# Optimization experiments

Measured on AMD Instinct MI355X. Metric: run time of the kernel, lower is better.

Reference implementation:

```python
import jax, jax.numpy as jnp
import numpy as np

BATCH = 4096
IN_CAPS = 64
OUT_CAPS = 16
IN_DIM = 64
OUT_DIM = 64
NUM_ITER = 3
LN_EPS = 1e-5


def setup_inputs() -> dict:
    key = jax.random.key(0)
    ks = jax.random.split(key, 13)
    n = lambda k, s: jax.random.normal(k, s, dtype=jnp.float32)
    return {
        "x_inp": n(ks[0], (BATCH, IN_CAPS, IN_DIM)),
        "W_A": n(ks[1], (IN_CAPS, IN_DIM)),
        "B_A": n(ks[2], (IN_CAPS,)),
        "W_F1": n(ks[3], (IN_CAPS, IN_DIM, IN_DIM)),
        "W_F2": n(ks[4], (OUT_CAPS, IN_DIM, OUT_DIM)),
        "B_F2": n(ks[5], (OUT_CAPS, OUT_DIM)),
        "W_G1": n(ks[6], (OUT_DIM, OUT_DIM)),
        "W_G2": n(ks[7], (OUT_CAPS, OUT_DIM, IN_DIM)),
        "B_G2": n(ks[8], (OUT_CAPS, IN_DIM)),
        "ln_gamma": jnp.ones((OUT_DIM,), jnp.float32),
        "ln_beta": jnp.zeros((OUT_DIM,), jnp.float32),
        "W_S": n(ks[9], (IN_CAPS, OUT_CAPS, IN_DIM)),
        "B_S": n(ks[10], (IN_CAPS, OUT_CAPS)),
        "beta_use": n(ks[11], (IN_CAPS, OUT_CAPS)),
        "beta_ign": n(ks[12], (IN_CAPS, OUT_CAPS)),
    }


def _layer_norm(x, gamma, beta):
    mu = jnp.mean(x, axis=-1, keepdims=True)
    var = jnp.var(x, axis=-1, keepdims=True)  # biased, matches torch LayerNorm
    return (x - mu) * jax.lax.rsqrt(var + LN_EPS) * gamma + beta


def reference(x_inp, W_A, B_A, W_F1, W_F2, B_F2, W_G1, W_G2, B_G2,
              ln_gamma, ln_beta, W_S, B_S, beta_use, beta_ign):
    B = x_inp.shape[0]
    inv_sqrt = np.float32(1.0 / np.sqrt(IN_DIM))
    # activation logits per input capsule: [B, in_caps]
    a_e = jnp.einsum('bif,if->bi', x_inp, W_A) * inv_sqrt + B_A
    f_a_e = jax.nn.sigmoid(a_e)  # loop-invariant
    # temp_F is loop-invariant: [B, in_caps, in_dim]
    temp_F = jnp.einsum('bif,ifh->bih', x_inp, W_F1) * inv_sqrt
    R_em = jnp.full((B, IN_CAPS, OUT_CAPS), 1.0 / OUT_CAPS, dtype=x_inp.dtype)
    x_out = None
    for _ in range(NUM_ITER):
        D_use = f_a_e[:, :, None] * R_em                      # [B,i,m]
        D_ign = f_a_e[:, :, None] - D_use                     # [B,i,m]
        phi_em = beta_use * D_use - beta_ign * D_ign          # [B,i,m]
        temp_F_routed = phi_em.sum(axis=-1)[:, :, None] * temp_F  # [B,i,h]
        x_out = jnp.einsum('bih,mhd->bmd', temp_F_routed, W_F2) + B_F2  # [B,m,d]
        x_out_norm = _layer_norm(x_out, ln_gamma, ln_beta)
        temp_G = jnp.einsum('bmd,dh->bmh', x_out_norm, W_G1)  # [B,m,d]
        x_inp_hat = jnp.einsum('bmh,mhi->bmi', temp_G, W_G2) + B_G2  # [B,m,f]
        consistency = jnp.einsum('bif,bmf,imf->bim', x_inp, x_inp_hat, W_S) + B_S
        R_em = jax.nn.softmax(consistency, axis=-1)  # exp(log_softmax)
    return x_out
```

## Files before the change

kernel.cpp:

```cpp
#include <hip/hip_runtime.h>
#include <math.h>

#define IC 64
#define OC 16
#define DIM 64

typedef __attribute__((ext_vector_type(8))) short bf16x8;
typedef __attribute__((ext_vector_type(4))) float f32x4;

__device__ __forceinline__ unsigned short f2bf(float f) {
    unsigned int b = __float_as_uint(f);
    b += 0x7fffu + ((b >> 16) & 1u);
    return (unsigned short)(b >> 16);
}
__device__ __forceinline__ float bf2f(unsigned short h) {
    return __uint_as_float(((unsigned int)h) << 16);
}

__global__ __launch_bounds__(256, 4)
void kF1(const float* __restrict__ W_F2, const float* __restrict__ W_S,
         const float* __restrict__ B_S, const float* __restrict__ bu,
         const float* __restrict__ bi_, const float* __restrict__ W_G1,
         const float* __restrict__ W_G2, const float* __restrict__ W_F1,
         const float* __restrict__ x, const float* __restrict__ W_A,
         const float* __restrict__ B_A,
         float* __restrict__ WSt2,
         unsigned short* __restrict__ W1h, unsigned short* __restrict__ W1l,
         unsigned short* __restrict__ W2h, unsigned short* __restrict__ W2l,
         unsigned short* __restrict__ WF1Th, unsigned short* __restrict__ WF1Tl,
         float* __restrict__ BSt, float* __restrict__ cb, float* __restrict__ db,
         float* __restrict__ xq, float* __restrict__ fa, float* __restrict__ phi)
{
    if (blockIdx.x < 256) {
        int e = blockIdx.x * 256 + threadIdx.x;
        {
            int h = e >> 10, m = (e >> 6) & 15, d = e & 63;
            float v = W_F2[((size_t)m * 64 + h) * 64 + d];
            unsigned short hh = f2bf(v);
            size_t o = ((size_t)m * 64 + d) * 64 + h;
            W1h[o] = hh; W1l[o] = f2bf(v - bf2f(hh));
        }
        {
            int m = e >> 12, fo = (e >> 8) & 15, i = (e >> 2) & 63, fi = e & 3;
            WSt2[e] = W_S[((size_t)i * 16 + m) * 64 + fo * 4 + fi];
        }
        {
            int m = e >> 12, d = (e >> 6) & 63, f = e & 63;
            const float* g1 = W_G1 + d * 64;
            const float* g2 = W_G2 + (size_t)m * 4096 + f;
            float a = 0.f;
#pragma unroll 8
            for (int h = 0; h < 64; h++) a += g1[h] * g2[h * 64];
            unsigned short hh = f2bf(a);
            size_t o = ((size_t)m * 64 + f) * 64 + d;
            W2h[o] = hh; W2l[o] = f2bf(a - bf2f(hh));
        }
        {
#pragma unroll
            for (int r = 0; r < 4; r++) {
                int idx = r * 65536 + e;
                int i = idx >> 12, h = (idx >> 6) & 63, f = idx & 63;
                float v = W_F1[(((size_t)i * 64 + f) * 64) + h];
                unsigned short hh = f2bf(v);
                size_t o = ((size_t)i * 64 + h) * 64 + f;
                WF1Th[o] = hh; WF1Tl[o] = f2bf(v - bf2f(hh));
            }
        }
        if (e < 1024) {
            int m = e >> 6, i = e & 63;
            BSt[e] = B_S[i * 16 + m];
            cb[e] = bu[e] + bi_[e];
        }
        if (e < 64) {
            float sd = 0.f;
            for (int m = 0; m < 16; m++) sd += bi_[e * 16 + m];
            db[e] = sd;
        }
        return;
    }

    __shared__ float Xs[2 * 64 * 65];
    const int t = threadIdx.x;
    const int blk = blockIdx.x - 256;

    const float4* x4 = (const float4*)x;
#pragma unroll
    for (int s = 0; s < 8; s++) {
        int p = s * 256 + t;
        float4 v = x4[(size_t)blk * 2048 + p];
        int b = p >> 10, i = (p >> 4) & 63, fo = p & 15;
        float* row = &Xs[(b * 64 + i) * 65 + fo * 4];
        row[0] = v.x; row[1] = v.y; row[2] = v.z; row[3] = v.w;
    }
    __syncthreads();

    const int lane = t & 63, w = t >> 6;
#pragma unroll
    for (int s = 0; s < 8; s++) {
        int idx = s * 4 + w;
        int b = idx >> 4, fo = idx & 15;
        const float* row = &Xs[(b * 64 + lane) * 65 + fo * 4];
        ((float4*)xq)[((size_t)(blk * 2 + b) * 16 + fo) * 64 + lane] =
            make_float4(row[0], row[1], row[2], row[3]);
    }

    {
        int p = t >> 1, h = t & 1;
        int b = p >> 6, i = p & 63;
        const float* row = &Xs[(b * 64 + i) * 65 + h * 32];
        const float* wa = W_A + i * 64 + h * 32;
        float v = 0.f;
#pragma unroll
        for (int j = 0; j < 32; j++) v += row[j] * wa[j];
        v += __shfl_xor(v, 1);
        if (h == 0) {
            float sc = 0.f, sd = 0.f;
            for (int m = 0; m < 16; m++) {
                float vu = bu[i * 16 + m], vi = bi_[i * 16 + m];
                sc += vu + vi; sd += vi;
            }
            float ebi = sc * (1.0f / 16.0f) - sd;
            float ae = v * 0.125f + B_A[i];
            float fv = 1.0f / (1.0f + expf(-ae));
            size_t o = (size_t)(blk * 2 + b) * 64 + i;
            fa[o] = fv;
            phi[o] = fv * ebi;
        }
    }
}

__global__ __launch_bounds__(256, 4)
void kA(const float* __restrict__ x,
        const unsigned short* __restrict__ WF1Th, const unsigned short* __restrict__ WF1Tl,
        float* __restrict__ tF)
{
    __shared__ unsigned short Ah[64][72], Al[64][72];
    __shared__ unsigned short Bh[64][72], Bl[64][72];
    const int i = blockIdx.y;
    const int b0 = blockIdx.x * 64;
    const int t = threadIdx.x;
    const int bl = t >> 2, q = t & 3;

    {
        const float* src = x + ((size_t)(b0 + bl) * IC + i) * DIM + q * 4;
#pragma unroll
        for (int j4 = 0; j4 < 4; j4++) {
            float4 v = *(const float4*)(src + j4 * 16);
            int f = q * 4 + j4 * 16;
            float vv[4] = {v.x, v.y, v.z, v.w};
            ushort4 h4, l4;
            unsigned short hh;
            hh = f2bf(vv[0]); h4.x = hh; l4.x = f2bf(vv[0] - bf2f(hh));
            hh = f2bf(vv[1]); h4.y = hh; l4.y = f2bf(vv[1] - bf2f(hh));
            hh = f2bf(vv[2]); h4.z = hh; l4.z = f2bf(vv[2] - bf2f(hh));
            hh = f2bf(vv[3]); h4.w = hh; l4.w = f2bf(vv[3] - bf2f(hh));
            *(ushort4*)&Ah[bl][f] = h4;
            *(ushort4*)&Al[bl][f] = l4;
        }
        const size_t wo = ((size_t)i * 64 + bl) * 64 + q * 16;
#pragma unroll
        for (int part = 0; part < 2; part++) {
            *(uint4*)&Bh[bl][q * 16 + part * 8] = *(const uint4*)(WF1Th + wo + part * 8);
            *(uint4*)&Bl[bl][q * 16 + part * 8] = *(const uint4*)(WF1Tl + wo + part * 8);
        }
    }
    __syncthreads();

    const int w = t >> 6, lane = t & 63;
    const int fm = lane & 15, fq = lane >> 4;
    const int r0 = w * 16;
    f32x4 acc[4];
#pragma unroll
    for (int nt = 0; nt < 4; nt++) {
        acc[nt][0] = 0.f; acc[nt][1] = 0.f; acc[nt][2] = 0.f; acc[nt][3] = 0.f;
    }

#pragma unroll
    for (int ks = 0; ks < 2; ks++) {
        const int kk = ks * 32 + fq * 8;
        bf16x8 ah = *(const bf16x8*)&Ah[r0 + fm][kk];
        bf16x8 al = *(const bf16x8*)&Al[r0 + fm][kk];
#pragma unroll
        for (int nt = 0; nt < 4; nt++) {
            bf16x8 bh = *(const bf16x8*)&Bh[nt * 16 + fm][kk];
            bf16x8 bl2 = *(const bf16x8*)&Bl[nt * 16 + fm][kk];
            acc[nt] = __builtin_amdgcn_mfma_f32_16x16x32_bf16(ah, bh, acc[nt], 0, 0, 0);
            acc[nt] = __builtin_amdgcn_mfma_f32_16x16x32_bf16(ah, bl2, acc[nt], 0, 0, 0);
            acc[nt] = __builtin_amdgcn_mfma_f32_16x16x32_bf16(al, bh, acc[nt], 0, 0, 0);
        }
    }

#pragma unroll
    for (int nt = 0; nt < 4; nt++)
#pragma unroll
        for (int j = 0; j < 4; j++) {
            int row = r0 + fq * 4 + j;
            int col = nt * 16 + fm;
            tF[((size_t)(b0 + row) * IC + i) * DIM + col] = acc[nt][j] * 0.125f;
        }
}

__global__ __launch_bounds__(256, 4)
void kS(const float* __restrict__ phi, const float* __restrict__ tF,
        float* __restrict__ s)
{
    __shared__ float ph[4 * 64];
    const int t = threadIdx.x;
    const int b0 = blockIdx.x * 4;
    ph[t] = phi[(size_t)b0 * 64 + t];
    __syncthreads();

    const int w = t >> 6, lane = t & 63;
    const int ig = lane >> 4, hq = lane & 15;
    const int b = b0 + w;
    const float4* tf4 = (const float4*)(tF + ((size_t)b * 64 + ig * 16) * 64) + hq;
    float4 a = make_float4(0.f, 0.f, 0.f, 0.f);
#pragma unroll
    for (int k = 0; k < 16; k++) {
        float p = ph[w * 64 + ig * 16 + k];
        float4 v = tf4[k * 16];
        a.x += p * v.x; a.y += p * v.y; a.z += p * v.z; a.w += p * v.w;
    }
#pragma unroll
    for (int k = 16; k <= 32; k <<= 1) {
        a.x += __shfl_xor(a.x, k); a.y += __shfl_xor(a.y, k);
        a.z += __shfl_xor(a.z, k); a.w += __shfl_xor(a.w, k);
    }
    if (ig == 0)
        ((float4*)(s + (size_t)b * 64))[hq] = a;
}

__global__ __launch_bounds__(256, 4)
void kXG(const float* __restrict__ s,
         const unsigned short* __restrict__ W1h, const unsigned short* __restrict__ W1l,
         const float* __restrict__ B_F2,
         const unsigned short* __restrict__ W2h, const unsigned short* __restrict__ W2l,
         const float* __restrict__ B_G2,
         const float* __restrict__ gam, const float* __restrict__ bet,
         float* __restrict__ xhat, float* __restrict__ out, const int last)
{
    __shared__ unsigned short Ah[64][72], Al[64][72];
    __shared__ unsigned short Bh[64][72], Bl[64][72];
    const int b0 = blockIdx.x * 64;
    const int m = blockIdx.y;
    const int t = threadIdx.x;
    const int bl = t >> 2, q = t & 3;

    {
        const float* src = s + (size_t)(b0 + bl) * DIM + q * 16;
#pragma unroll
        for (int j4 = 0; j4 < 4; j4++) {
            float4 v = ((const float4*)src)[j4];
            int f = q * 16 + j4 * 4;
            float vv[4] = {v.x, v.y, v.z, v.w};
            ushort4 h4, l4;
            unsigned short hh;
            hh = f2bf(vv[0]); h4.x = hh; l4.x = f2bf(vv[0] - bf2f(hh));
            hh = f2bf(vv[1]); h4.y = hh; l4.y = f2bf(vv[1] - bf2f(hh));
            hh = f2bf(vv[2]); h4.z = hh; l4.z = f2bf(vv[2] - bf2f(hh));
            hh = f2bf(vv[3]); h4.w = hh; l4.w = f2bf(vv[3] - bf2f(hh));
            *(ushort4*)&Ah[bl][f] = h4;
            *(ushort4*)&Al[bl][f] = l4;
        }
        const size_t wo = ((size_t)m * 64 + bl) * 64 + q * 16;
#pragma unroll
        for (int part = 0; part < 2; part++) {
            *(uint4*)&Bh[bl][q * 16 + part * 8] = *(const uint4*)(W1h + wo + part * 8);
            *(uint4*)&Bl[bl][q * 16 + part * 8] = *(const uint4*)(W1l + wo + part * 8);
        }
    }
    __syncthreads();

    const int w = t >> 6, lane = t & 63;
    const int fm = lane & 15, fq = lane >> 4;
    const int r0 = w * 16;
    f32x4 acc[4];
#pragma unroll
    for (int nt = 0; nt < 4; nt++) {
        acc[nt][0] = 0.f; acc[nt][1] = 0.f; acc[nt][2] = 0.f; acc[nt][3] = 0.f;
    }
#pragma unroll
    for (int ks = 0; ks < 2; ks++) {
        const int kk = ks * 32 + fq * 8;
        bf16x8 ah = *(const bf16x8*)&Ah[r0 + fm][kk];
        bf16x8 al = *(const bf16x8*)&Al[r0 + fm][kk];
#pragma unroll
        for (int nt = 0; nt < 4; nt++) {
            bf16x8 bh = *(const bf16x8*)&Bh[nt * 16 + fm][kk];
            bf16x8 bl2 = *(const bf16x8*)&Bl[nt * 16 + fm][kk];
            acc[nt] = __builtin_amdgcn_mfma_f32_16x16x32_bf16(ah, bh, acc[nt], 0, 0, 0);
            acc[nt] = __builtin_amdgcn_mfma_f32_16x16x32_bf16(ah, bl2, acc[nt], 0, 0, 0);
            acc[nt] = __builtin_amdgcn_mfma_f32_16x16x32_bf16(al, bh, acc[nt], 0, 0, 0);
        }
    }
#pragma unroll
    for (int nt = 0; nt < 4; nt++) {
        float bf = B_F2[m * DIM + nt * 16 + fm];
#pragma unroll
        for (int j = 0; j < 4; j++) acc[nt][j] += bf;
    }

    if (last) {
#pragma unroll
        for (int nt = 0; nt < 4; nt++)
#pragma unroll
            for (int j = 0; j < 4; j++) {
                int row = r0 + fq * 4 + j;
                out[((size_t)(b0 + row) * OC + m) * DIM + nt * 16 + fm] = acc[nt][j];
            }
        return;
    }

    {
        float g4[4], b4[4];
#pragma unroll
        for (int nt = 0; nt < 4; nt++) {
            g4[nt] = gam[nt * 16 + fm];
            b4[nt] = bet[nt * 16 + fm];
        }
#pragma unroll
        for (int j = 0; j < 4; j++) {
            float sum = acc[0][j] + acc[1][j] + acc[2][j] + acc[3][j];
            float sq = acc[0][j] * acc[0][j] + acc[1][j] * acc[1][j] +
                       acc[2][j] * acc[2][j] + acc[3][j] * acc[3][j];
#pragma unroll
            for (int k = 1; k <= 8; k <<= 1) {
                sum += __shfl_xor(sum, k);
                sq  += __shfl_xor(sq, k);
            }
            float mu = sum * (1.0f / 64.0f);
            float var = sq * (1.0f / 64.0f) - mu * mu;
            float rs = 1.0f / sqrtf(var + 1e-5f);
#pragma unroll
            for (int nt = 0; nt < 4; nt++)
                acc[nt][j] = (acc[nt][j] - mu) * rs * g4[nt] + b4[nt];
        }
    }
    __syncthreads();

    {
#pragma unroll
        for (int nt = 0; nt < 4; nt++)
#pragma unroll
            for (int j = 0; j < 4; j++) {
                float v = acc[nt][j];
                unsigned short hh = f2bf(v);
                int row = r0 + fq * 4 + j, col = nt * 16 + fm;
                Ah[row][col] = hh;
                Al[row][col] = f2bf(v - bf2f(hh));
            }
        const size_t wo = ((size_t)m * 64 + bl) * 64 + q * 16;
#pragma unroll
        for (int part = 0; part < 2; part++) {
            *(uint4*)&Bh[bl][q * 16 + part * 8] = *(const uint4*)(W2h + wo + part * 8);
            *(uint4*)&Bl[bl][q * 16 + part * 8] = *(const uint4*)(W2l + wo + part * 8);
        }
    }
    __syncthreads();

    f32x4 xh[4];
#pragma unroll
    for (int nt = 0; nt < 4; nt++) {
        float bg = B_G2[m * DIM + nt * 16 + fm];
        xh[nt][0] = bg; xh[nt][1] = bg; xh[nt][2] = bg; xh[nt][3] = bg;
    }
#pragma unroll
    for (int ks = 0; ks < 2; ks++) {
        const int kk = ks * 32 + fq * 8;
        bf16x8 ah = *(const bf16x8*)&Ah[r0 + fm][kk];
        bf16x8 al = *(const bf16x8*)&Al[r0 + fm][kk];
#pragma unroll
        for (int nt = 0; nt < 4; nt++) {
            bf16x8 bh = *(const bf16x8*)&Bh[nt * 16 + fm][kk];
            bf16x8 bl2 = *(const bf16x8*)&Bl[nt * 16 + fm][kk];
            xh[nt] = __builtin_amdgcn_mfma_f32_16x16x32_bf16(ah, bh, xh[nt], 0, 0, 0);
            xh[nt] = __builtin_amdgcn_mfma_f32_16x16x32_bf16(ah, bl2, xh[nt], 0, 0, 0);
            xh[nt] = __builtin_amdgcn_mfma_f32_16x16x32_bf16(al, bh, xh[nt], 0, 0, 0);
        }
    }
#pragma unroll
    for (int nt = 0; nt < 4; nt++)
#pragma unroll
        for (int j = 0; j < 4; j++) {
            int row = r0 + fq * 4 + j;
            xhat[((size_t)(b0 + row) * OC + m) * DIM + nt * 16 + fm] = xh[nt][j];
        }
}

__global__ __launch_bounds__(256, 4)
void kC(const float* __restrict__ xq, const float* __restrict__ xhat,
        const float* __restrict__ WSt2, const float* __restrict__ BSt,
        const float* __restrict__ cb, const float* __restrict__ db,
        const float* __restrict__ fa, const float* __restrict__ tF,
        float* __restrict__ s)
{
    __shared__ float buf[4 * 64 * 17];
    __shared__ float phs[4][64];
    const int b0 = blockIdx.x * 4;
    const int t = threadIdx.x;
    const int w = t >> 6, lane = t & 63;

    {
        const float4* src = (const float4*)(xhat + (size_t)b0 * OC * DIM);
        float4* dst = (float4*)buf;
#pragma unroll
        for (int j = 0; j < 4; j++) dst[t + j * 256] = src[t + j * 256];
    }
    __syncthreads();

    float acc[4][4];
#pragma unroll
    for (int k = 0; k < 4; k++) {
        float bs = BSt[(w * 4 + k) * IC + lane];
#pragma unroll
        for (int g = 0; g < 4; g++) acc[g][k] = bs;
    }

    const float4* xq4 = (const float4*)xq;
    for (int fc = 0; fc < 64; fc += 8) {
        const int fo = fc >> 2;
        float wreg[4][8];
#pragma unroll
        for (int k = 0; k < 4; k++) {
            int m = w * 4 + k;
#pragma unroll
            for (int q2 = 0; q2 < 2; q2++) {
                float4 v = *(const float4*)&WSt2[(((size_t)m * 16 + fo + q2) * IC + lane) * 4];
                wreg[k][q2 * 4 + 0] = v.x; wreg[k][q2 * 4 + 1] = v.y;
                wreg[k][q2 * 4 + 2] = v.z; wreg[k][q2 * 4 + 3] = v.w;
            }
        }
#pragma unroll
        for (int g = 0; g < 4; g++) {
            float xr[8];
#pragma unroll
            for (int q2 = 0; q2 < 2; q2++) {
                float4 v = xq4[((size_t)(b0 + g) * 16 + fo + q2) * 64 + lane];
                xr[q2 * 4 + 0] = v.x; xr[q2 * 4 + 1] = v.y;
                xr[q2 * 4 + 2] = v.z; xr[q2 * 4 + 3] = v.w;
            }
#pragma unroll
            for (int k = 0; k < 4; k++) {
                int m = w * 4 + k;
                const float* hp = &buf[(g * OC + m) * DIM + fc];
                float hr[8];
#pragma unroll
                for (int q2 = 0; q2 < 2; q2++) {
                    float4 v = *(const float4*)(hp + q2 * 4);
                    hr[q2 * 4 + 0] = v.x; hr[q2 * 4 + 1] = v.y;
                    hr[q2 * 4 + 2] = v.z; hr[q2 * 4 + 3] = v.w;
                }
#pragma unroll
                for (int ff = 0; ff < 8; ff++)
                    acc[g][k] += xr[ff] * hr[ff] * wreg[k][ff];
            }
        }
    }
    __syncthreads();
#pragma unroll
    for (int g = 0; g < 4; g++)
#pragma unroll
        for (int k = 0; k < 4; k++)
            buf[(g * IC + lane) * 17 + w * 4 + k] = acc[g][k];
    __syncthreads();

    {
        int g = t >> 6, i = t & 63;
        const float* row = &buf[(g * IC + i) * 17];
        float v[16], mx = -1e30f;
#pragma unroll
        for (int m = 0; m < OC; m++) { v[m] = row[m]; mx = fmaxf(mx, v[m]); }
        float sum = 0.f;
#pragma unroll
        for (int m = 0; m < OC; m++) { v[m] = expf(v[m] - mx); sum += v[m]; }
        float inv = 1.0f / sum;
        float a2 = 0.f;
#pragma unroll
        for (int m = 0; m < OC; m++) a2 += v[m] * inv * cb[i * OC + m];
        phs[g][i] = fa[(size_t)(b0 + g) * IC + i] * (a2 - db[i]);
    }
    __syncthreads();

    {
        const int ig = lane >> 4, hq = lane & 15;
        const int b = b0 + w;
        const float4* tf4 = (const float4*)(tF + ((size_t)b * 64 + ig * 16) * 64) + hq;
        float4 a = make_float4(0.f, 0.f, 0.f, 0.f);
#pragma unroll
        for (int k = 0; k < 16; k++) {
            float p = phs[w][ig * 16 + k];
            float4 v = tf4[k * 16];
            a.x += p * v.x; a.y += p * v.y; a.z += p * v.z; a.w += p * v.w;
        }
#pragma unroll
        for (int k = 16; k <= 32; k <<= 1) {
            a.x += __shfl_xor(a.x, k); a.y += __shfl_xor(a.y, k);
            a.z += __shfl_xor(a.z, k); a.w += __shfl_xor(a.w, k);
        }
        if (ig == 0)
            ((float4*)(s + (size_t)b * 64))[hq] = a;
    }
}

extern "C" void kernel_launch(void* const* d_in, const int* in_sizes, int n_in,
                              void* d_out, int out_size, void* d_ws, size_t ws_size,
                              hipStream_t stream)
{
    const float* x    = (const float*)d_in[0];
    const float* W_A  = (const float*)d_in[1];
    const float* B_A  = (const float*)d_in[2];
    const float* W_F1 = (const float*)d_in[3];
    const float* W_F2 = (const float*)d_in[4];
    const float* B_F2 = (const float*)d_in[5];
    const float* W_G1 = (const float*)d_in[6];
    const float* W_G2 = (const float*)d_in[7];
    const float* B_G2 = (const float*)d_in[8];
    const float* gam  = (const float*)d_in[9];
    const float* bet  = (const float*)d_in[10];
    const float* W_S  = (const float*)d_in[11];
    const float* B_S  = (const float*)d_in[12];
    const float* bu   = (const float*)d_in[13];
    const float* bi_  = (const float*)d_in[14];

    float* ws   = (float*)d_ws;
    float* tF   = ws;
    float* xq   = tF + 16777216;
    float* fa   = xq + 16777216;
    float* phi  = fa + 262144;
    float* s    = phi + 262144;
    float* xhat = s + 262144;
    float* WSt2 = xhat + 4194304;
    unsigned short* W1h = (unsigned short*)(WSt2 + 65536);
    unsigned short* W1l = W1h + 65536;
    unsigned short* W2h = W1l + 65536;
    unsigned short* W2l = W2h + 65536;
    float* BSt  = (float*)(W2l + 65536);
    float* cb   = BSt + 1024;
    float* db   = cb + 1024;
    unsigned short* WF1Th = (unsigned short*)(db + 64);
    unsigned short* WF1Tl = WF1Th + 262144;
    float* out  = (float*)d_out;

    kF1<<<2304, 256, 0, stream>>>(W_F2, W_S, B_S, bu, bi_, W_G1, W_G2, W_F1,
                                  x, W_A, B_A,
                                  WSt2, W1h, W1l, W2h, W2l, WF1Th, WF1Tl,
                                  BSt, cb, db, xq, fa, phi);
    kA<<<dim3(64, 64), 256, 0, stream>>>(x, WF1Th, WF1Tl, tF);
    kS<<<1024, 256, 0, stream>>>(phi, tF, s);
    for (int it = 0; it < 3; ++it) {
        kXG<<<dim3(64, 16), 256, 0, stream>>>(s, W1h, W1l, B_F2, W2h, W2l, B_G2,
                                              gam, bet, xhat, out, it == 2 ? 1 : 0);
        if (it < 2)
            kC<<<1024, 256, 0, stream>>>(xq, xhat, WSt2, BSt, cb, db, fa, tF, s);
    }
}
```

Measured before the change: 279.3 us.

## Fuse temp_F GEMM into prep kernel and split W_F1 inline

The separate kA launch is folded into kF1 as extra blocks, which now use a shared raw LDS buffer. The W_F1 transposed bf16 hi/lo split that kF1 precomputed into a workspace is dropped. Each GEMM block instead loads W_F1 fp32 directly and splits and transposes it into LDS. This removes one kernel launch, the W_F1 workspace round-trip, and the dependency between the weight prep and the GEMM. In exchange each GEMM block redoes the conversion, the transposed LDS stores may bank-conflict, and the larger static shared allocation may lower occupancy for the non-GEMM blocks.

```diff
diff --git a/kernel.cpp b/kernel.cpp
--- a/kernel.cpp
+++ b/kernel.cpp
@@ -27,12 +27,16 @@
          float* __restrict__ WSt2,
          unsigned short* __restrict__ W1h, unsigned short* __restrict__ W1l,
          unsigned short* __restrict__ W2h, unsigned short* __restrict__ W2l,
-         unsigned short* __restrict__ WF1Th, unsigned short* __restrict__ WF1Tl,
          float* __restrict__ BSt, float* __restrict__ cb, float* __restrict__ db,
-         float* __restrict__ xq, float* __restrict__ fa, float* __restrict__ phi)
+         float* __restrict__ xq, float* __restrict__ fa, float* __restrict__ phi,
+         float* __restrict__ tF)
 {
-    if (blockIdx.x < 256) {
-        int e = blockIdx.x * 256 + threadIdx.x;
+    __shared__ __align__(16) unsigned char raw[36864];
+    const int bx = blockIdx.x;
+    const int t = threadIdx.x;
+
+    if (bx < 256) {
+        int e = bx * 256 + t;
         {
             int h = e >> 10, m = (e >> 6) & 15, d = e & 63;
             float v = W_F2[((size_t)m * 64 + h) * 64 + d];
@@ -55,17 +59,6 @@
             size_t o = ((size_t)m * 64 + f) * 64 + d;
             W2h[o] = hh; W2l[o] = f2bf(a - bf2f(hh));
         }
-        {
-#pragma unroll
-            for (int r = 0; r < 4; r++) {
-                int idx = r * 65536 + e;
-                int i = idx >> 12, h = (idx >> 6) & 63, f = idx & 63;
-                float v = W_F1[(((size_t)i * 64 + f) * 64) + h];
-                unsigned short hh = f2bf(v);
-                size_t o = ((size_t)i * 64 + h) * 64 + f;
-                WF1Th[o] = hh; WF1Tl[o] = f2bf(v - bf2f(hh));
-            }
-        }
         if (e < 1024) {
             int m = e >> 6, i = e & 63;
             BSt[e] = B_S[i * 16 + m];
@@ -79,125 +72,132 @@
         return;
     }
 
-    __shared__ float Xs[2 * 64 * 65];
-    const int t = threadIdx.x;
-    const int blk = blockIdx.x - 256;
-
-    const float4* x4 = (const float4*)x;
-#pragma unroll
-    for (int s = 0; s < 8; s++) {
-        int p = s * 256 + t;
-        float4 v = x4[(size_t)blk * 2048 + p];
-        int b = p >> 10, i = (p >> 4) & 63, fo = p & 15;
-        float* row = &Xs[(b * 64 + i) * 65 + fo * 4];
-        row[0] = v.x; row[1] = v.y; row[2] = v.z; row[3] = v.w;
-    }
-    __syncthreads();
-
-    const int lane = t & 63, w = t >> 6;
-#pragma unroll
-    for (int s = 0; s < 8; s++) {
-        int idx = s * 4 + w;
-        int b = idx >> 4, fo = idx & 15;
-        const float* row = &Xs[(b * 64 + lane) * 65 + fo * 4];
-        ((float4*)xq)[((size_t)(blk * 2 + b) * 16 + fo) * 64 + lane] =
-            make_float4(row[0], row[1], row[2], row[3]);
-    }
-
-    {
-        int p = t >> 1, h = t & 1;
-        int b = p >> 6, i = p & 63;
-        const float* row = &Xs[(b * 64 + i) * 65 + h * 32];
-        const float* wa = W_A + i * 64 + h * 32;
-        float v = 0.f;
-#pragma unroll
-        for (int j = 0; j < 32; j++) v += row[j] * wa[j];
-        v += __shfl_xor(v, 1);
-        if (h == 0) {
-            float sc = 0.f, sd = 0.f;
-            for (int m = 0; m < 16; m++) {
-                float vu = bu[i * 16 + m], vi = bi_[i * 16 + m];
-                sc += vu + vi; sd += vi;
-            }
-            float ebi = sc * (1.0f / 16.0f) - sd;
-            float ae = v * 0.125f + B_A[i];
-            float fv = 1.0f / (1.0f + expf(-ae));
-            size_t o = (size_t)(blk * 2 + b) * 64 + i;
-            fa[o] = fv;
-            phi[o] = fv * ebi;
-        }
-    }
-}
-
-__global__ __launch_bounds__(256, 4)
-void kA(const float* __restrict__ x,
-        const unsigned short* __restrict__ WF1Th, const unsigned short* __restrict__ WF1Tl,
-        float* __restrict__ tF)
-{
-    __shared__ unsigned short Ah[64][72], Al[64][72];
-    __shared__ unsigned short Bh[64][72], Bl[64][72];
-    const int i = blockIdx.y;
-    const int b0 = blockIdx.x * 64;
-    const int t = threadIdx.x;
-    const int bl = t >> 2, q = t & 3;
-
-    {
-        const float* src = x + ((size_t)(b0 + bl) * IC + i) * DIM + q * 4;
-#pragma unroll
-        for (int j4 = 0; j4 < 4; j4++) {
-            float4 v = *(const float4*)(src + j4 * 16);
-            int f = q * 4 + j4 * 16;
-            float vv[4] = {v.x, v.y, v.z, v.w};
-            ushort4 h4, l4;
-            unsigned short hh;
-            hh = f2bf(vv[0]); h4.x = hh; l4.x = f2bf(vv[0] - bf2f(hh));
-            hh = f2bf(vv[1]); h4.y = hh; l4.y = f2bf(vv[1] - bf2f(hh));
-            hh = f2bf(vv[2]); h4.z = hh; l4.z = f2bf(vv[2] - bf2f(hh));
-            hh = f2bf(vv[3]); h4.w = hh; l4.w = f2bf(vv[3] - bf2f(hh));
-            *(ushort4*)&Ah[bl][f] = h4;
-            *(ushort4*)&Al[bl][f] = l4;
-        }
-        const size_t wo = ((size_t)i * 64 + bl) * 64 + q * 16;
-#pragma unroll
-        for (int part = 0; part < 2; part++) {
-            *(uint4*)&Bh[bl][q * 16 + part * 8] = *(const uint4*)(WF1Th + wo + part * 8);
-            *(uint4*)&Bl[bl][q * 16 + part * 8] = *(const uint4*)(WF1Tl + wo + part * 8);
-        }
-    }
-    __syncthreads();
-
-    const int w = t >> 6, lane = t & 63;
-    const int fm = lane & 15, fq = lane >> 4;
-    const int r0 = w * 16;
-    f32x4 acc[4];
-#pragma unroll
-    for (int nt = 0; nt < 4; nt++) {
-        acc[nt][0] = 0.f; acc[nt][1] = 0.f; acc[nt][2] = 0.f; acc[nt][3] = 0.f;
-    }
-
-#pragma unroll
-    for (int ks = 0; ks < 2; ks++) {
-        const int kk = ks * 32 + fq * 8;
-        bf16x8 ah = *(const bf16x8*)&Ah[r0 + fm][kk];
-        bf16x8 al = *(const bf16x8*)&Al[r0 + fm][kk];
+    if (bx < 2304) {
+        float* Xs = (float*)raw;
+        const int blk = bx - 256;
+
+        const float4* x4 = (const float4*)x;
+#pragma unroll
+        for (int s = 0; s < 8; s++) {
+            int p = s * 256 + t;
+            float4 v = x4[(size_t)blk * 2048 + p];
+            int b = p >> 10, i = (p >> 4) & 63, fo = p & 15;
+            float* row = &Xs[(b * 64 + i) * 65 + fo * 4];
+            row[0] = v.x; row[1] = v.y; row[2] = v.z; row[3] = v.w;
+        }
+        __syncthreads();
+
+        const int lane = t & 63, w = t >> 6;
+#pragma unroll
+        for (int s = 0; s < 8; s++) {
+            int idx = s * 4 + w;
+            int b = idx >> 4, fo = idx & 15;
+            const float* row = &Xs[(b * 64 + lane) * 65 + fo * 4];
+            ((float4*)xq)[((size_t)(blk * 2 + b) * 16 + fo) * 64 + lane] =
+                make_float4(row[0], row[1], row[2], row[3]);
+        }
+
+        {
+            int p = t >> 1, h = t & 1;
+            int b = p >> 6, i = p & 63;
+            const float* row = &Xs[(b * 64 + i) * 65 + h * 32];
+            const float* wa = W_A + i * 64 + h * 32;
+            float v = 0.f;
+#pragma unroll
+            for (int j = 0; j < 32; j++) v += row[j] * wa[j];
+            v += __shfl_xor(v, 1);
+            if (h == 0) {
+                float sc = 0.f, sd = 0.f;
+                for (int m = 0; m < 16; m++) {
+                    float vu = bu[i * 16 + m], vi = bi_[i * 16 + m];
+                    sc += vu + vi; sd += vi;
+                }
+                float ebi = sc * (1.0f / 16.0f) - sd;
+                float ae = v * 0.125f + B_A[i];
+                float fv = 1.0f / (1.0f + expf(-ae));
+                size_t o = (size_t)(blk * 2 + b) * 64 + i;
+                fa[o] = fv;
+                phi[o] = fv * ebi;
+            }
+        }
+        return;
+    }
+
+    {
+        unsigned short* Ah = (unsigned short*)raw;
+        unsigned short* Al = Ah + 64 * 72;
+        unsigned short* Bh = Al + 64 * 72;
+        unsigned short* Bl = Bh + 64 * 72;
+        const int ba = bx - 2304;
+        const int b0 = (ba & 63) * 64;
+        const int i = ba >> 6;
+        const int bl = t >> 2, q = t & 3;
+
+        {
+            const float* src = x + ((size_t)(b0 + bl) * IC + i) * DIM + q * 4;
+#pragma unroll
+            for (int j4 = 0; j4 < 4; j4++) {
+                float4 v = *(const float4*)(src + j4 * 16);
+                int f = q * 4 + j4 * 16;
+                float vv[4] = {v.x, v.y, v.z, v.w};
+                ushort4 h4, l4;
+                unsigned short hh;
+                hh = f2bf(vv[0]); h4.x = hh; l4.x = f2bf(vv[0] - bf2f(hh));
+                hh = f2bf(vv[1]); h4.y = hh; l4.y = f2bf(vv[1] - bf2f(hh));
+                hh = f2bf(vv[2]); h4.z = hh; l4.z = f2bf(vv[2] - bf2f(hh));
+                hh = f2bf(vv[3]); h4.w = hh; l4.w = f2bf(vv[3] - bf2f(hh));
+                *(ushort4*)&Ah[bl * 72 + f] = h4;
+                *(ushort4*)&Al[bl * 72 + f] = l4;
+            }
+            const float* wsrc = W_F1 + ((size_t)i * DIM + bl) * DIM + q * 4;
+#pragma unroll
+            for (int j4 = 0; j4 < 4; j4++) {
+                float4 v = *(const float4*)(wsrc + j4 * 16);
+                int h0 = q * 4 + j4 * 16;
+                float vv[4] = {v.x, v.y, v.z, v.w};
+#pragma unroll
+                for (int c = 0; c < 4; c++) {
+                    unsigned short hh = f2bf(vv[c]);
+                    Bh[(h0 + c) * 72 + bl] = hh;
+                    Bl[(h0 + c) * 72 + bl] = f2bf(vv[c] - bf2f(hh));
+                }
+            }
+        }
+        __syncthreads();
+
+        const int w = t >> 6, lane = t & 63;
+        const int fm = lane & 15, fq = lane >> 4;
+        const int r0 = w * 16;
+        f32x4 acc[4];
 #pragma unroll
         for (int nt = 0; nt < 4; nt++) {
-            bf16x8 bh = *(const bf16x8*)&Bh[nt * 16 + fm][kk];
-            bf16x8 bl2 = *(const bf16x8*)&Bl[nt * 16 + fm][kk];
-            acc[nt] = __builtin_amdgcn_mfma_f32_16x16x32_bf16(ah, bh, acc[nt], 0, 0, 0);
-            acc[nt] = __builtin_amdgcn_mfma_f32_16x16x32_bf16(ah, bl2, acc[nt], 0, 0, 0);
-            acc[nt] = __builtin_amdgcn_mfma_f32_16x16x32_bf16(al, bh, acc[nt], 0, 0, 0);
-        }
-    }
-
-#pragma unroll
-    for (int nt = 0; nt < 4; nt++)
-#pragma unroll
-        for (int j = 0; j < 4; j++) {
-            int row = r0 + fq * 4 + j;
-            int col = nt * 16 + fm;
-            tF[((size_t)(b0 + row) * IC + i) * DIM + col] = acc[nt][j] * 0.125f;
-        }
+            acc[nt][0] = 0.f; acc[nt][1] = 0.f; acc[nt][2] = 0.f; acc[nt][3] = 0.f;
+        }
+
+#pragma unroll
+        for (int ks = 0; ks < 2; ks++) {
+            const int kk = ks * 32 + fq * 8;
+            bf16x8 ah = *(const bf16x8*)&Ah[(r0 + fm) * 72 + kk];
+            bf16x8 al = *(const bf16x8*)&Al[(r0 + fm) * 72 + kk];
+#pragma unroll
+            for (int nt = 0; nt < 4; nt++) {
+                bf16x8 bh = *(const bf16x8*)&Bh[(nt * 16 + fm) * 72 + kk];
+                bf16x8 bl2 = *(const bf16x8*)&Bl[(nt * 16 + fm) * 72 + kk];
+                acc[nt] = __builtin_amdgcn_mfma_f32_16x16x32_bf16(ah, bh, acc[nt], 0, 0, 0);
+                acc[nt] = __builtin_amdgcn_mfma_f32_16x16x32_bf16(ah, bl2, acc[nt], 0, 0, 0);
+                acc[nt] = __builtin_amdgcn_mfma_f32_16x16x32_bf16(al, bh, acc[nt], 0, 0, 0);
+            }
+        }
+
+#pragma unroll
+        for (int nt = 0; nt < 4; nt++)
+#pragma unroll
+            for (int j = 0; j < 4; j++) {
+                int row = r0 + fq * 4 + j;
+                int col = nt * 16 + fm;
+                tF[((size_t)(b0 + row) * IC + i) * DIM + col] = acc[nt][j] * 0.125f;
+            }
+    }
 }
 
 __global__ __launch_bounds__(256, 4)
@@ -537,15 +537,12 @@
     float* BSt  = (float*)(W2l + 65536);
     float* cb   = BSt + 1024;
     float* db   = cb + 1024;
-    unsigned short* WF1Th = (unsigned short*)(db + 64);
-    unsigned short* WF1Tl = WF1Th + 262144;
     float* out  = (float*)d_out;
 
-    kF1<<<2304, 256, 0, stream>>>(W_F2, W_S, B_S, bu, bi_, W_G1, W_G2, W_F1,
+    kF1<<<6400, 256, 0, stream>>>(W_F2, W_S, B_S, bu, bi_, W_G1, W_G2, W_F1,
                                   x, W_A, B_A,
-                                  WSt2, W1h, W1l, W2h, W2l, WF1Th, WF1Tl,
-                                  BSt, cb, db, xq, fa, phi);
-    kA<<<dim3(64, 64), 256, 0, stream>>>(x, WF1Th, WF1Tl, tF);
+                                  WSt2, W1h, W1l, W2h, W2l,
+                                  BSt, cb, db, xq, fa, phi, tF);
     kS<<<1024, 256, 0, stream>>>(phi, tF, s);
     for (int it = 0; it < 3; ++it) {
         kXG<<<dim3(64, 16), 256, 0, stream>>>(s, W1h, W1l, B_F2, W2h, W2l, B_G2,
```

Result: no change. 275.2 us, median of 2 (-1.5%).
